# Performance work log

Measured on AMD Instinct MI355X. Metric: run time of the kernel, lower is better.

Reference implementation:

```python
import jax, jax.numpy as jnp
import numpy as np

B, L, D = 4, 2048, 512
H, DK, DV = 8, 64, 64


def setup_inputs() -> dict:
    key = jax.random.key(0)
    ks = jax.random.split(key, 12)
    s = 0.02
    return {
        "query": jax.random.normal(ks[0], (B, L, D), jnp.float32),
        "key": jax.random.normal(ks[1], (B, L, D), jnp.float32),
        "value": jax.random.normal(ks[2], (B, L, D), jnp.float32),
        "attention_mask": jax.random.normal(ks[3], (1, 1, L, L), jnp.float32),
        "Wq": jax.random.normal(ks[4], (D, H * DK), jnp.float32) * s,
        "bq": jnp.zeros((H * DK,), jnp.float32),
        "Wk": jax.random.normal(ks[5], (D, H * DK), jnp.float32) * s,
        "bk": jnp.zeros((H * DK,), jnp.float32),
        "Wv": jax.random.normal(ks[6], (D, H * DV), jnp.float32) * s,
        "bv": jnp.zeros((H * DV,), jnp.float32),
        "Wo": jax.random.normal(ks[7], (H * DV, D), jnp.float32) * s,
        "bo": jnp.zeros((D,), jnp.float32),
    }


def reference(query, key, value, attention_mask, Wq, bq, Wk, bk, Wv, bv, Wo, bo):
    sz_b, len_q, _ = query.shape
    len_k = key.shape[1]
    # projections -> [B, L, H, d]
    q = (query @ Wq + bq).reshape(sz_b, len_q, H, DK)
    k = (key @ Wk + bk).reshape(sz_b, len_k, H, DK)
    v = (value @ Wv + bv).reshape(sz_b, len_k, H, DV)
    # permute(2,0,1,3): heads first -> [H, B, L, d]
    q = jnp.transpose(q, (2, 0, 1, 3))
    k = jnp.transpose(k, (2, 0, 1, 3))
    v = jnp.transpose(v, (2, 0, 1, 3))
    scale = 1.0 / jnp.sqrt(jnp.asarray(DK, q.dtype))
    scores = jnp.einsum('hbqd,hbkd->hbqk', q, k) * scale + attention_mask
    attn = jax.nn.softmax(scores, axis=-1)
    x = jnp.einsum('hbqk,hbkd->hbqd', attn, v)  # [H, B, Lq, Dv]
    # faithful to torch: transpose(1,2) -> [H, Lq, B, Dv] then view(B, Lq, H*Dv)
    x = jnp.transpose(x, (0, 2, 1, 3)).reshape(sz_b, len_q, H * DV)
    return x @ Wo + bo
```

## Files before the change

### kernel.cpp

```cpp
#include <hip/hip_runtime.h>

#define SEQ    2048
#define DMODEL 512
#define NHEAD  8
#define HDIM   64
#define BATCH  4
#define NROWS  65536
#define KSPLIT 2

#define LOG2E  1.4426950408889634f
#define QSCALE 0.18033688011112042f

typedef float f32x4  __attribute__((ext_vector_type(4)));
typedef float f32x16 __attribute__((ext_vector_type(16)));
typedef _Float16 h16x8 __attribute__((ext_vector_type(8)));
typedef _Float16 h16x2 __attribute__((ext_vector_type(2)));
typedef unsigned int u32x2 __attribute__((ext_vector_type(2)));

union U4H { uint4 u; h16x8 h; };
union U1H2 { unsigned int u; h16x2 h; };

static __device__ inline h16x2 pkrtz(float a, float b) {
    return __builtin_bit_cast(h16x2, __builtin_amdgcn_cvt_pkrtz(a, b));
}
static __device__ inline unsigned short f2h(float x) {
    _Float16 h = (_Float16)x;
    return __builtin_bit_cast(unsigned short, h);
}
static __device__ inline void async_cp16(const void* g, void* l) {
    __builtin_amdgcn_global_load_lds(
        (const __attribute__((address_space(1))) unsigned int*)g,
        (__attribute__((address_space(3))) unsigned int*)l,
        16, 0, 0);
}

__global__ __launch_bounds__(256) void transpose_cast_w(
    const float* __restrict__ s0, const float* __restrict__ s1,
    const float* __restrict__ s2, const float* __restrict__ s3,
    unsigned short* __restrict__ d0, unsigned short* __restrict__ d1,
    unsigned short* __restrict__ d2, unsigned short* __restrict__ d3)
{
    const float* S; unsigned short* D;
    switch (blockIdx.z) {
        case 0: S = s0; D = d0; break;
        case 1: S = s1; D = d1; break;
        case 2: S = s2; D = d2; break;
        default: S = s3; D = d3; break;
    }
    __shared__ float T[32][33];
    const int t = threadIdx.x;
    const int r = t >> 3, c = (t & 7) * 4;
    const int k0 = blockIdx.x * 32, n0 = blockIdx.y * 32;
    float4 v = *(const float4*)&S[(size_t)(k0 + r) * DMODEL + n0 + c];
    T[r][c] = v.x; T[r][c + 1] = v.y; T[r][c + 2] = v.z; T[r][c + 3] = v.w;
    __syncthreads();
    ushort4 o;
    o.x = f2h(T[c + 0][r]); o.y = f2h(T[c + 1][r]);
    o.z = f2h(T[c + 2][r]); o.w = f2h(T[c + 3][r]);
    *(ushort4*)&D[(size_t)(n0 + r) * DMODEL + k0 + c] = o;
}

__global__ __launch_bounds__(256) void prep_mask(
    const float* __restrict__ mask, unsigned short* __restrict__ mp)
{
    int i = blockIdx.x * 256 + threadIdx.x;
    int k = (i * 4) & (SEQ - 1);
    int q = (i * 4) >> 11;
    float4 v = ((const float4*)mask)[i];
    int kt = k >> 6, kl = k & 63;
    int mt = kl >> 5, g = (kl >> 3) & 3, hl = (kl >> 2) & 1;
    size_t base = ((size_t)kt * SEQ + q) * 64 + hl * 32 + mt * 16 + g * 4;
    ushort4 o;
    o.x = f2h(__builtin_amdgcn_exp2f(v.x * LOG2E));
    o.y = f2h(__builtin_amdgcn_exp2f(v.y * LOG2E));
    o.z = f2h(__builtin_amdgcn_exp2f(v.z * LOG2E));
    o.w = f2h(__builtin_amdgcn_exp2f(v.w * LOG2E));
    *(ushort4*)&mp[base] = o;
}

__global__ __launch_bounds__(256) void cast_a16(
    const float* __restrict__ s0, const float* __restrict__ s1,
    const float* __restrict__ s2,
    unsigned short* __restrict__ d0, unsigned short* __restrict__ d1,
    unsigned short* __restrict__ d2)
{
    const float* S; unsigned short* D;
    switch (blockIdx.z) {
        case 0: S = s0; D = d0; break;
        case 1: S = s1; D = d1; break;
        default: S = s2; D = d2; break;
    }
    size_t i = ((size_t)blockIdx.x * 256 + threadIdx.x) * 8;
    float4 a = *(const float4*)&S[i];
    float4 b = *(const float4*)&S[i + 4];
    U1H2 p0, p1, p2, p3;
    p0.h = pkrtz(a.x, a.y); p1.h = pkrtz(a.z, a.w);
    p2.h = pkrtz(b.x, b.y); p3.h = pkrtz(b.z, b.w);
    *(uint4*)&D[i] = make_uint4(p0.u, p1.u, p2.u, p3.u);
}

template <int EPI>
static __device__ inline void gemm_core16(
    const unsigned short* __restrict__ Ab, const unsigned short* __restrict__ Bt,
    const float* __restrict__ bias, void* __restrict__ Cout, float oscale,
    int bm, int bn)
{
    __shared__ __align__(16) unsigned short As[2][128 * 32];
    __shared__ __align__(16) unsigned short Bs[2][128 * 32];

    const int t = threadIdx.x;
    const int lane = t & 63, w = t >> 6;
    const int wm = w >> 1, wn = w & 1;
    const int c = lane & 15, quad = lane >> 4;
    const int srow = lane >> 2;
    const int sck  = (lane & 3) ^ ((lane >> 3) & 3);

    f32x4 acc[4][4] = {};

    #pragma unroll
    for (int i = 0; i < 2; i++) {
        int row = 32 * w + 16 * i + srow;
        async_cp16(Ab + (size_t)(bm + row) * DMODEL + sck * 8,
                   &As[0][(32 * w + 16 * i) * 32]);
        async_cp16(Bt + (size_t)(bn + row) * DMODEL + sck * 8,
                   &Bs[0][(32 * w + 16 * i) * 32]);
    }
    __syncthreads();

    const int slot8 = (quad ^ ((c >> 1) & 3)) * 8;

    for (int k0 = 0; k0 < DMODEL; k0 += 32) {
        const int cur = (k0 >> 5) & 1;
        if (k0 + 32 < DMODEL) {
            #pragma unroll
            for (int i = 0; i < 2; i++) {
                int row = 32 * w + 16 * i + srow;
                async_cp16(Ab + (size_t)(bm + row) * DMODEL + k0 + 32 + sck * 8,
                           &As[cur ^ 1][(32 * w + 16 * i) * 32]);
                async_cp16(Bt + (size_t)(bn + row) * DMODEL + k0 + 32 + sck * 8,
                           &Bs[cur ^ 1][(32 * w + 16 * i) * 32]);
            }
        }
        U4H af[4], bf[4];
        #pragma unroll
        for (int mt = 0; mt < 4; mt++)
            af[mt].u = *(const uint4*)&As[cur][(wm * 64 + mt * 16 + c) * 32 + slot8];
        #pragma unroll
        for (int nt = 0; nt < 4; nt++)
            bf[nt].u = *(const uint4*)&Bs[cur][(wn * 64 + nt * 16 + c) * 32 + slot8];
        #pragma unroll
        for (int mt = 0; mt < 4; mt++)
            #pragma unroll
            for (int nt = 0; nt < 4; nt++)
                acc[mt][nt] = __builtin_amdgcn_mfma_f32_16x16x32_f16(
                    af[mt].h, bf[nt].h, acc[mt][nt], 0, 0, 0);
        __syncthreads();
    }

    if (EPI == 2) {
        #pragma unroll
        for (int nt = 0; nt < 4; nt++) {
            int ng = bn + wn * 64 + nt * 16 + c;
            int h = ng >> 6, dv = ng & 63;
            float bv = bias[ng];
            #pragma unroll
            for (int mt = 0; mt < 4; mt++) {
                int mg0 = bm + wm * 64 + mt * 16 + quad * 4;
                int bb = mg0 >> 11, key0 = mg0 & (SEQ - 1);
                U1H2 lo, hi;
                lo.h = pkrtz(acc[mt][nt][0] + bv, acc[mt][nt][1] + bv);
                hi.h = pkrtz(acc[mt][nt][2] + bv, acc[mt][nt][3] + bv);
                *(uint2*)&((unsigned short*)Cout)[
                    ((size_t)(bb * NHEAD + h) * HDIM + dv) * SEQ + key0] =
                    make_uint2(lo.u, hi.u);
            }
        }
        return;
    }
    #pragma unroll
    for (int nt = 0; nt < 4; nt++) {
        int ng = bn + wn * 64 + nt * 16 + c;
        float bv = bias[ng];
        #pragma unroll
        for (int mt = 0; mt < 4; mt++) {
            #pragma unroll
            for (int r = 0; r < 4; r++) {
                int mg = bm + wm * 64 + mt * 16 + quad * 4 + r;
                float v = (acc[mt][nt][r] + bv) * oscale;
                if (EPI == 1)
                    ((unsigned short*)Cout)[(size_t)mg * DMODEL + ng] = f2h(v);
                else
                    ((float*)Cout)[(size_t)mg * DMODEL + ng] = v;
            }
        }
    }
}

struct QKVArgs {
    const unsigned short *A0, *A1, *A2;
    const unsigned short *W0, *W1, *W2;
    const float *b0, *b1, *b2;
    unsigned short *o0, *o1, *o2;
};

__global__ __launch_bounds__(256) void gemm_qkv(QKVArgs a) {
    if (blockIdx.z == 2)
        gemm_core16<2>(a.A2, a.W2, a.b2, a.o2, 1.0f, blockIdx.y * 128, blockIdx.x * 128);
    else if (blockIdx.z == 1)
        gemm_core16<1>(a.A1, a.W1, a.b1, a.o1, 1.0f, blockIdx.y * 128, blockIdx.x * 128);
    else
        gemm_core16<1>(a.A0, a.W0, a.b0, a.o0, QSCALE, blockIdx.y * 128, blockIdx.x * 128);
}

__global__ __launch_bounds__(256) void gemm_fin(
    const unsigned short* __restrict__ A, const unsigned short* __restrict__ W,
    const float* __restrict__ bias, float* __restrict__ C) {
    gemm_core16<0>(A, W, bias, C, 1.0f, blockIdx.y * 128, blockIdx.x * 128);
}

__global__ __launch_bounds__(256, 3) void attn5(
    const unsigned short* __restrict__ qb, const unsigned short* __restrict__ kb,
    const unsigned short* __restrict__ vT, const unsigned short* __restrict__ emp,
    unsigned short* __restrict__ Xp, float* __restrict__ Lp)
{
    __shared__ __align__(16) unsigned short Ks[2][64 * 64];
    __shared__ __align__(16) unsigned short Vs[2][64 * 64];

    const int t = threadIdx.x;
    const int lane = t & 63, w = t >> 6;
    const int c32 = lane & 31, hl = lane >> 5;
    const int bh = blockIdx.x, b = bh >> 3, head = bh & 7;
    const int q0 = blockIdx.y * 128;
    const int split = blockIdx.z;
    const int qg = q0 + w * 32 + c32;

    const unsigned short* qrow = qb + ((size_t)b * SEQ + qg) * DMODEL + head * HDIM;
    U4H Qf[4];
    #pragma unroll
    for (int s = 0; s < 4; s++)
        Qf[s].u = *(const uint4*)&qrow[s * 16 + hl * 8];

    const unsigned short* kgb = kb + (size_t)b * SEQ * DMODEL + head * HDIM
                              + (size_t)split * 1024 * DMODEL;
    const unsigned short* vgb = vT + (size_t)bh * HDIM * SEQ + split * 1024;

    const int srow = lane >> 3;
    const int sch  = (lane & 7) ^ srow;

    {
        #pragma unroll
        for (int i = 0; i < 2; i++) {
            int row = w * 16 + i * 8 + srow;
            async_cp16(&kgb[(size_t)row * DMODEL + sch * 8], &Ks[0][(w * 16 + i * 8) * 64]);
            async_cp16(&vgb[(size_t)row * SEQ + sch * 8],    &Vs[0][(w * 16 + i * 8) * 64]);
        }
    }

    U4H e0, e1, e2, e3;
    {
        const unsigned short* mrow = emp + ((size_t)(split * 16) * SEQ + qg) * 64 + hl * 32;
        e0.u = *(const uint4*)&mrow[0];
        e1.u = *(const uint4*)&mrow[8];
        e2.u = *(const uint4*)&mrow[16];
        e3.u = *(const uint4*)&mrow[24];
    }

    f32x16 O0 = {}, O1 = {};
    float lsum = 0.f;
    const h16x2 one2 = {(_Float16)1.0f, (_Float16)1.0f};

    for (int kt = 0; kt < 1024 / 64; kt++) {
        const int p = kt & 1;
        __syncthreads();

        if (kt + 1 < 1024 / 64) {
            int k0n = (kt + 1) * 64;
            #pragma unroll
            for (int i = 0; i < 2; i++) {
                int row = w * 16 + i * 8 + srow;
                async_cp16(&kgb[(size_t)(k0n + row) * DMODEL + sch * 8],
                           &Ks[p ^ 1][(w * 16 + i * 8) * 64]);
                async_cp16(&vgb[(size_t)row * SEQ + k0n + sch * 8],
                           &Vs[p ^ 1][(w * 16 + i * 8) * 64]);
            }
        }

        U4H f0, f1, f2, f3;
        {
            int ktn = (kt + 1 < 1024 / 64) ? kt + 1 : kt;
            const unsigned short* mrow =
                emp + ((size_t)(split * 16 + ktn) * SEQ + qg) * 64 + hl * 32;
            f0.u = *(const uint4*)&mrow[0];
            f1.u = *(const uint4*)&mrow[8];
            f2.u = *(const uint4*)&mrow[16];
            f3.u = *(const uint4*)&mrow[24];
        }

        const unsigned short* Kp = Ks[p];
        const unsigned short* Vp = Vs[p];

        f32x16 S0 = {}, S1 = {};
        __builtin_amdgcn_s_setprio(1);
        #pragma unroll
        for (int s = 0; s < 4; s++) {
            int fc = 2 * s + hl;
            int sl = (fc ^ (c32 & 7)) * 8;
            U4H ka0, ka1;
            ka0.u = *(const uint4*)&Kp[c32 * 64 + sl];
            ka1.u = *(const uint4*)&Kp[(32 + c32) * 64 + sl];
            S0 = __builtin_amdgcn_mfma_f32_32x32x16_f16(ka0.h, Qf[s].h, S0, 0, 0, 0);
            S1 = __builtin_amdgcn_mfma_f32_32x32x16_f16(ka1.h, Qf[s].h, S1, 0, 0, 0);
        }
        __builtin_amdgcn_s_setprio(0);

        unsigned int Pf[4][4];
        #pragma unroll
        for (int mt = 0; mt < 2; mt++) {
            f32x16 S = mt ? S1 : S0;
            h16x8 ea = (mt ? e2 : e0).h;
            h16x8 eb = (mt ? e3 : e1).h;
            unsigned int u[4][2];
            #pragma unroll
            for (int jj = 0; jj < 8; jj++) {
                _Float16 exl = (jj < 4) ? ea[2 * jj]     : eb[2 * jj - 8];
                _Float16 exh = (jj < 4) ? ea[2 * jj + 1] : eb[2 * jj - 7];
                h16x2 ex = {exl, exh};
                h16x2 pk = pkrtz(__builtin_amdgcn_exp2f(S[2 * jj]),
                                 __builtin_amdgcn_exp2f(S[2 * jj + 1]));
                h16x2 pp = pk * ex;
#if __has_builtin(__builtin_amdgcn_fdot2)
                lsum = __builtin_amdgcn_fdot2(pp, one2, lsum, false);
#else
                lsum += (float)pp[0] + (float)pp[1];
#endif
                u[jj >> 1][jj & 1] = __builtin_bit_cast(unsigned int, pp);
            }
#if __has_builtin(__builtin_amdgcn_permlane32_swap)
            u32x2 rA0 = __builtin_amdgcn_permlane32_swap(u[0][0], u[1][0], false, false);
            u32x2 rA1 = __builtin_amdgcn_permlane32_swap(u[0][1], u[1][1], false, false);
            u32x2 rB0 = __builtin_amdgcn_permlane32_swap(u[2][0], u[3][0], false, false);
            u32x2 rB1 = __builtin_amdgcn_permlane32_swap(u[2][1], u[3][1], false, false);
            Pf[2 * mt + 0][0] = rA0[0]; Pf[2 * mt + 0][1] = rA1[0];
            Pf[2 * mt + 0][2] = rA0[1]; Pf[2 * mt + 0][3] = rA1[1];
            Pf[2 * mt + 1][0] = rB0[0]; Pf[2 * mt + 1][1] = rB1[0];
            Pf[2 * mt + 1][2] = rB0[1]; Pf[2 * mt + 1][3] = rB1[1];
#else
            unsigned int sA0 = hl ? u[0][0] : u[1][0];
            unsigned int sA1 = hl ? u[0][1] : u[1][1];
            unsigned int sB0 = hl ? u[2][0] : u[3][0];
            unsigned int sB1 = hl ? u[2][1] : u[3][1];
            unsigned int rA0 = (unsigned)__shfl_xor((int)sA0, 32, 64);
            unsigned int rA1 = (unsigned)__shfl_xor((int)sA1, 32, 64);
            unsigned int rB0 = (unsigned)__shfl_xor((int)sB0, 32, 64);
            unsigned int rB1 = (unsigned)__shfl_xor((int)sB1, 32, 64);
            Pf[2 * mt + 0][0] = hl ? rA0 : u[0][0];
            Pf[2 * mt + 0][1] = hl ? rA1 : u[0][1];
            Pf[2 * mt + 0][2] = hl ? u[1][0] : rA0;
            Pf[2 * mt + 0][3] = hl ? u[1][1] : rA1;
            Pf[2 * mt + 1][0] = hl ? rB0 : u[2][0];
            Pf[2 * mt + 1][1] = hl ? rB1 : u[2][1];
            Pf[2 * mt + 1][2] = hl ? u[3][0] : rB0;
            Pf[2 * mt + 1][3] = hl ? u[3][1] : rB1;
#endif
        }

        __builtin_amdgcn_s_setprio(1);
        #pragma unroll
        for (int s = 0; s < 4; s++) {
            int kc = 2 * s + hl;
            int sl = (kc ^ (c32 & 7)) * 8;
            U4H va0, va1, pu;
            va0.u = *(const uint4*)&Vp[c32 * 64 + sl];
            va1.u = *(const uint4*)&Vp[(32 + c32) * 64 + sl];
            pu.u = make_uint4(Pf[s][0], Pf[s][1], Pf[s][2], Pf[s][3]);
            O0 = __builtin_amdgcn_mfma_f32_32x32x16_f16(va0.h, pu.h, O0, 0, 0, 0);
            O1 = __builtin_amdgcn_mfma_f32_32x32x16_f16(va1.h, pu.h, O1, 0, 0, 0);
        }
        __builtin_amdgcn_s_setprio(0);

        e0 = f0; e1 = f1; e2 = f2; e3 = f3;
    }

    lsum += __shfl_xor(lsum, 32, 64);
    const size_t j = ((size_t)head * SEQ + qg) * BATCH + b;
    unsigned short* xr = Xp + ((size_t)split * NROWS + j) * HDIM;
    #pragma unroll
    for (int mt = 0; mt < 2; mt++) {
        f32x16 Ov = mt ? O1 : O0;
        #pragma unroll
        for (int g = 0; g < 4; g++) {
            U1H2 lo, hi;
            lo.h = pkrtz(Ov[g * 4 + 0], Ov[g * 4 + 1]);
            hi.h = pkrtz(Ov[g * 4 + 2], Ov[g * 4 + 3]);
            uint2 st = make_uint2(lo.u, hi.u);
            *(uint2*)&xr[mt * 32 + 8 * g + 4 * hl] = st;
        }
    }
    if (hl == 0) Lp[split * NROWS + j] = lsum;
}

__global__ __launch_bounds__(256) void combine_attn(
    const unsigned short* __restrict__ Xp, const float* __restrict__ Lp,
    unsigned short* __restrict__ xb)
{
    int i = blockIdx.x * 256 + threadIdx.x;
    int j = i >> 3, dc = (i & 7) * 8;
    U4H a, b;
    a.u = *(const uint4*)&Xp[(size_t)j * HDIM + dc];
    b.u = *(const uint4*)&Xp[((size_t)NROWS + j) * HDIM + dc];
    float inv = 1.0f / (Lp[j] + Lp[NROWS + j]);
    U4H o;
    #pragma unroll
    for (int p = 0; p < 4; p++) {
        float s0 = ((float)a.h[2 * p]     + (float)b.h[2 * p])     * inv;
        float s1 = ((float)a.h[2 * p + 1] + (float)b.h[2 * p + 1]) * inv;
        h16x2 pk = pkrtz(s0, s1);
        o.h[2 * p] = pk[0]; o.h[2 * p + 1] = pk[1];
    }
    *(uint4*)&xb[(size_t)j * HDIM + dc] = o.u;
}

extern "C" void kernel_launch(void* const* d_in, const int* in_sizes, int n_in,
                              void* d_out, int out_size, void* d_ws, size_t ws_size,
                              hipStream_t stream) {
    const float* query = (const float*)d_in[0];
    const float* key_  = (const float*)d_in[1];
    const float* value = (const float*)d_in[2];
    const float* mask  = (const float*)d_in[3];
    const float* Wq = (const float*)d_in[4];
    const float* bq = (const float*)d_in[5];
    const float* Wk = (const float*)d_in[6];
    const float* bk = (const float*)d_in[7];
    const float* Wv = (const float*)d_in[8];
    const float* bv = (const float*)d_in[9];
    const float* Wo = (const float*)d_in[10];
    const float* bo = (const float*)d_in[11];
    float* out = (float*)d_out;

    const size_t NP = (size_t)BATCH * SEQ * DMODEL;
    unsigned short* ws   = (unsigned short*)d_ws;
    unsigned short* qb16 = ws;
    unsigned short* kb16 = qb16 + NP;
    unsigned short* vT16 = kb16 + NP;
    unsigned short* xb16 = vT16 + NP;
    unsigned short* em16 = xb16 + NP;
    unsigned short* Xp16 = em16 + (size_t)SEQ * SEQ;
    unsigned short* WqT  = Xp16 + (size_t)KSPLIT * NROWS * HDIM;
    unsigned short* WkT  = WqT + DMODEL * DMODEL;
    unsigned short* WvT  = WkT + DMODEL * DMODEL;
    unsigned short* WoT  = WvT + DMODEL * DMODEL;
    float* Lp = (float*)(WoT + DMODEL * DMODEL);

    unsigned short* q16 = xb16;
    unsigned short* k16 = Xp16;
    unsigned short* v16 = Xp16 + NP;

    transpose_cast_w<<<dim3(16, 16, 4), 256, 0, stream>>>(
        Wq, Wk, Wv, Wo, WqT, WkT, WvT, WoT);
    prep_mask<<<dim3(SEQ * SEQ / 4 / 256), 256, 0, stream>>>(mask, em16);
    cast_a16<<<dim3(NP / 8 / 256, 1, 3), 256, 0, stream>>>(
        query, key_, value, q16, k16, v16);

    QKVArgs qa;
    qa.A0 = q16;  qa.A1 = k16;  qa.A2 = v16;
    qa.W0 = WqT;  qa.W1 = WkT;  qa.W2 = WvT;
    qa.b0 = bq;   qa.b1 = bk;   qa.b2 = bv;
    qa.o0 = qb16; qa.o1 = kb16; qa.o2 = vT16;
    gemm_qkv<<<dim3(DMODEL / 128, BATCH * SEQ / 128, 3), 256, 0, stream>>>(qa);

    attn5<<<dim3(BATCH * NHEAD, SEQ / 128, KSPLIT), 256, 0, stream>>>(
        qb16, kb16, vT16, em16, Xp16, Lp);

    combine_attn<<<dim3(NROWS * 8 / 256), 256, 0, stream>>>(Xp16, Lp, xb16);

    gemm_fin<<<dim3(DMODEL / 128, BATCH * SEQ / 128), 256, 0, stream>>>(
        xb16, WoT, bo, out);
}
```

Measured before the change: 235.7 us.

## Merge prep kernels into one launch and remap attention grid for XCD locality

Result: no change. 235.8 us (+0.0%).

```diff
diff --git a/kernel.cpp b/kernel.cpp
--- a/kernel.cpp
+++ b/kernel.cpp
@@ -34,69 +34,68 @@
         16, 0, 0);
 }
 
-__global__ __launch_bounds__(256) void transpose_cast_w(
-    const float* __restrict__ s0, const float* __restrict__ s1,
-    const float* __restrict__ s2, const float* __restrict__ s3,
-    unsigned short* __restrict__ d0, unsigned short* __restrict__ d1,
-    unsigned short* __restrict__ d2, unsigned short* __restrict__ d3)
-{
-    const float* S; unsigned short* D;
-    switch (blockIdx.z) {
-        case 0: S = s0; D = d0; break;
-        case 1: S = s1; D = d1; break;
-        case 2: S = s2; D = d2; break;
-        default: S = s3; D = d3; break;
-    }
-    __shared__ float T[32][33];
+struct PrepArgs {
+    const float *Wq, *Wk, *Wv, *Wo;
+    unsigned short *WqT, *WkT, *WvT, *WoT;
+    const float *mask; unsigned short *mp;
+    const float *aq, *ak, *av;
+    unsigned short *dq, *dk, *dv;
+};
+
+__global__ __launch_bounds__(256) void prepass(PrepArgs a) {
+    const int bid = blockIdx.x;
     const int t = threadIdx.x;
-    const int r = t >> 3, c = (t & 7) * 4;
-    const int k0 = blockIdx.x * 32, n0 = blockIdx.y * 32;
-    float4 v = *(const float4*)&S[(size_t)(k0 + r) * DMODEL + n0 + c];
-    T[r][c] = v.x; T[r][c + 1] = v.y; T[r][c + 2] = v.z; T[r][c + 3] = v.w;
-    __syncthreads();
-    ushort4 o;
-    o.x = f2h(T[c + 0][r]); o.y = f2h(T[c + 1][r]);
-    o.z = f2h(T[c + 2][r]); o.w = f2h(T[c + 3][r]);
-    *(ushort4*)&D[(size_t)(n0 + r) * DMODEL + k0 + c] = o;
-}
-
-__global__ __launch_bounds__(256) void prep_mask(
-    const float* __restrict__ mask, unsigned short* __restrict__ mp)
-{
-    int i = blockIdx.x * 256 + threadIdx.x;
-    int k = (i * 4) & (SEQ - 1);
-    int q = (i * 4) >> 11;
-    float4 v = ((const float4*)mask)[i];
-    int kt = k >> 6, kl = k & 63;
-    int mt = kl >> 5, g = (kl >> 3) & 3, hl = (kl >> 2) & 1;
-    size_t base = ((size_t)kt * SEQ + q) * 64 + hl * 32 + mt * 16 + g * 4;
-    ushort4 o;
-    o.x = f2h(__builtin_amdgcn_exp2f(v.x * LOG2E));
-    o.y = f2h(__builtin_amdgcn_exp2f(v.y * LOG2E));
-    o.z = f2h(__builtin_amdgcn_exp2f(v.z * LOG2E));
-    o.w = f2h(__builtin_amdgcn_exp2f(v.w * LOG2E));
-    *(ushort4*)&mp[base] = o;
-}
-
-__global__ __launch_bounds__(256) void cast_a16(
-    const float* __restrict__ s0, const float* __restrict__ s1,
-    const float* __restrict__ s2,
-    unsigned short* __restrict__ d0, unsigned short* __restrict__ d1,
-    unsigned short* __restrict__ d2)
-{
-    const float* S; unsigned short* D;
-    switch (blockIdx.z) {
-        case 0: S = s0; D = d0; break;
-        case 1: S = s1; D = d1; break;
-        default: S = s2; D = d2; break;
-    }
-    size_t i = ((size_t)blockIdx.x * 256 + threadIdx.x) * 8;
-    float4 a = *(const float4*)&S[i];
-    float4 b = *(const float4*)&S[i + 4];
-    U1H2 p0, p1, p2, p3;
-    p0.h = pkrtz(a.x, a.y); p1.h = pkrtz(a.z, a.w);
-    p2.h = pkrtz(b.x, b.y); p3.h = pkrtz(b.z, b.w);
-    *(uint4*)&D[i] = make_uint4(p0.u, p1.u, p2.u, p3.u);
+
+    if (bid < 1024) {
+        const int z = bid >> 8, y = (bid >> 4) & 15, x = bid & 15;
+        const float* S; unsigned short* D;
+        switch (z) {
+            case 0: S = a.Wq; D = a.WqT; break;
+            case 1: S = a.Wk; D = a.WkT; break;
+            case 2: S = a.Wv; D = a.WvT; break;
+            default: S = a.Wo; D = a.WoT; break;
+        }
+        __shared__ float T[32][33];
+        const int r = t >> 3, c = (t & 7) * 4;
+        const int k0 = x * 32, n0 = y * 32;
+        float4 v = *(const float4*)&S[(size_t)(k0 + r) * DMODEL + n0 + c];
+        T[r][c] = v.x; T[r][c + 1] = v.y; T[r][c + 2] = v.z; T[r][c + 3] = v.w;
+        __syncthreads();
+        ushort4 o;
+        o.x = f2h(T[c + 0][r]); o.y = f2h(T[c + 1][r]);
+        o.z = f2h(T[c + 2][r]); o.w = f2h(T[c + 3][r]);
+        *(ushort4*)&D[(size_t)(n0 + r) * DMODEL + k0 + c] = o;
+    } else if (bid < 1024 + 4096) {
+        int i = (bid - 1024) * 256 + t;
+        int k = (i * 4) & (SEQ - 1);
+        int q = (i * 4) >> 11;
+        float4 v = ((const float4*)a.mask)[i];
+        int kt = k >> 6, kl = k & 63;
+        int mt = kl >> 5, g = (kl >> 3) & 3, hl = (kl >> 2) & 1;
+        size_t base = ((size_t)kt * SEQ + q) * 64 + hl * 32 + mt * 16 + g * 4;
+        ushort4 o;
+        o.x = f2h(__builtin_amdgcn_exp2f(v.x * LOG2E));
+        o.y = f2h(__builtin_amdgcn_exp2f(v.y * LOG2E));
+        o.z = f2h(__builtin_amdgcn_exp2f(v.z * LOG2E));
+        o.w = f2h(__builtin_amdgcn_exp2f(v.w * LOG2E));
+        *(ushort4*)&a.mp[base] = o;
+    } else {
+        int u = bid - 5120;
+        int z = u >> 11, blk = u & 2047;
+        const float* S; unsigned short* D;
+        switch (z) {
+            case 0: S = a.aq; D = a.dq; break;
+            case 1: S = a.ak; D = a.dk; break;
+            default: S = a.av; D = a.dv; break;
+        }
+        size_t i = ((size_t)blk * 256 + t) * 8;
+        float4 x = *(const float4*)&S[i];
+        float4 y = *(const float4*)&S[i + 4];
+        U1H2 p0, p1, p2, p3;
+        p0.h = pkrtz(x.x, x.y); p1.h = pkrtz(x.z, x.w);
+        p2.h = pkrtz(y.x, y.y); p3.h = pkrtz(y.z, y.w);
+        *(uint4*)&D[i] = make_uint4(p0.u, p1.u, p2.u, p3.u);
+    }
 }
 
 template <int EPI>
@@ -229,9 +228,14 @@
     const int t = threadIdx.x;
     const int lane = t & 63, w = t >> 6;
     const int c32 = lane & 31, hl = lane >> 5;
-    const int bh = blockIdx.x, b = bh >> 3, head = bh & 7;
-    const int q0 = blockIdx.y * 128;
-    const int split = blockIdx.z;
+
+    const int bid = blockIdx.x;
+    const int xcd = bid & 7, slot = bid >> 3;
+    const int bh = slot & 31;
+    const int comb = (slot >> 5) * 8 + xcd;
+    const int split = comb >> 4;
+    const int q0 = (comb & 15) * 128;
+    const int b = bh >> 3, head = bh & 7;
     const int qg = q0 + w * 32 + c32;
 
     const unsigned short* qrow = qb + ((size_t)b * SEQ + qg) * DMODEL + head * HDIM;
@@ -455,11 +459,13 @@
     unsigned short* k16 = Xp16;
     unsigned short* v16 = Xp16 + NP;
 
-    transpose_cast_w<<<dim3(16, 16, 4), 256, 0, stream>>>(
-        Wq, Wk, Wv, Wo, WqT, WkT, WvT, WoT);
-    prep_mask<<<dim3(SEQ * SEQ / 4 / 256), 256, 0, stream>>>(mask, em16);
-    cast_a16<<<dim3(NP / 8 / 256, 1, 3), 256, 0, stream>>>(
-        query, key_, value, q16, k16, v16);
+    PrepArgs pa;
+    pa.Wq = Wq; pa.Wk = Wk; pa.Wv = Wv; pa.Wo = Wo;
+    pa.WqT = WqT; pa.WkT = WkT; pa.WvT = WvT; pa.WoT = WoT;
+    pa.mask = mask; pa.mp = em16;
+    pa.aq = query; pa.ak = key_; pa.av = value;
+    pa.dq = q16; pa.dk = k16; pa.dv = v16;
+    prepass<<<dim3(1024 + 4096 + 6144), 256, 0, stream>>>(pa);
 
     QKVArgs qa;
     qa.A0 = q16;  qa.A1 = k16;  qa.A2 = v16;
@@ -468,7 +474,7 @@
     qa.o0 = qb16; qa.o1 = kb16; qa.o2 = vT16;
     gemm_qkv<<<dim3(DMODEL / 128, BATCH * SEQ / 128, 3), 256, 0, stream>>>(qa);
 
-    attn5<<<dim3(BATCH * NHEAD, SEQ / 128, KSPLIT), 256, 0, stream>>>(
+    attn5<<<dim3(BATCH * NHEAD * (SEQ / 128) * KSPLIT), 256, 0, stream>>>(
         qb16, kb16, vT16, em16, Xp16, Lp);
 
     combine_attn<<<dim3(NROWS * 8 / 256), 256, 0, stream>>>(Xp16, Lp, xb16);
```
